# Performance work log

Measured on AMD Instinct MI355X. Metric: run time of the kernel, lower is better.

## Reference

```python
import jax, jax.numpy as jnp
import numpy as np

MAX_DISP = 40   # init kwarg max_disp
STRIDE_2 = 1    # init kwarg stride_2


def setup_inputs() -> dict:
    key = jax.random.key(0)
    k1, k2 = jax.random.split(key)
    B, C, H, W = 8, 128, 160, 320
    x_1 = jax.random.normal(k1, (B, C, H, W), dtype=jnp.float32)
    x_2 = jax.random.normal(k2, (B, C, H, W), dtype=jnp.float32)
    return {"x_1": x_1, "x_2": x_2}


def reference(x_1, x_2):
    # x_1, x_2: [B, C, H, W]
    pad = MAX_DISP * 2
    W = x_1.shape[3]
    # left-pad x_2 along width, matching F.pad(x_2, (pad, 0, 0, 0))
    x2p = jnp.pad(x_2, ((0, 0), (0, 0), (0, 0), (pad, 0)))
    # one [B,H,W] correlation map per displacement (small fixed set of 81 shifts)
    outs = [
        jnp.sum(x_1 * jax.lax.dynamic_slice_in_dim(x2p, d, W, axis=3), axis=1)
        for d in range(0, pad + 1, STRIDE_2)
    ]
    return jnp.stack(outs, axis=1)  # [B, D, H, W], D = 2*max_disp//stride + 1
```

## Files before the change

kernel.cpp:

```cpp
#include <hip/hip_runtime.h>


#define CB 8
#define CC 128
#define CH 160
#define CW 320
#define CD 81
#define CPAD 80
#define TW 160
#define NTHR 640
#define AROWS 160
#define BROWS 240
#define KC 64
#define ROWP 72
#define HW (CH*CW)

typedef __attribute__((ext_vector_type(8))) short short8;
typedef __attribute__((ext_vector_type(4))) float f32x4;

__device__ __forceinline__ unsigned pk2(float a, float b) {
    unsigned ua = __float_as_uint(a), ub = __float_as_uint(b);
    ua = (ua + 0x7fffu + ((ua >> 16) & 1u)) >> 16;
    ub = (ub + 0x7fffu + ((ub >> 16) & 1u)) >> 16;
    return ua | (ub << 16);
}

__global__ __launch_bounds__(NTHR, 5) void corr1d_mfma(
    const float* __restrict__ x1,
    const float* __restrict__ x2,
    float* __restrict__ out)
{
    __shared__ __align__(16) unsigned short lA[AROWS * ROWP];
    __shared__ __align__(16) unsigned short lB[BROWS * ROWP];

    const int tid = threadIdx.x;
    const int bid = blockIdx.x;
    const int wt = bid & 1;
    const int h  = (bid >> 1) % CH;
    const int b  = bid / (2 * CH);
    const int w0 = wt * TW;

    const int lane = tid & 63;
    const int s    = tid >> 6;
    const int n    = lane & 15;
    const int q    = lane >> 4;

    const float* x1p = x1 + ((size_t)b * CC * CH + (size_t)h) * CW;
    const float* x2p = x2 + ((size_t)b * CC * CH + (size_t)h) * CW;

    f32x4 acc[6];
#pragma unroll
    for (int t = 0; t < 6; t++) acc[t] = (f32x4){0.f, 0.f, 0.f, 0.f};

    for (int c0 = 0; c0 < CC; c0 += KC) {
        if (c0) __syncthreads();

#pragma unroll
        for (int j = 0; j < 3; j++) {
            int i = tid + j * NTHR;
            if (i < 1600) {
                int cq = i & 15;
                int rt = i >> 4;
                int kl = cq << 2;
                int c  = c0 + kl;
                float4 v[4];
                unsigned short* dst;
                if (rt < 40) {
                    int gw = w0 + (rt << 2);
                    const float* p = x1p + (size_t)c * HW + gw;
#pragma unroll
                    for (int cc = 0; cc < 4; cc++)
                        v[cc] = *(const float4*)(p + (size_t)cc * HW);
                    dst = &lA[(rt << 2) * ROWP + kl];
                } else {
                    int rb = rt - 40;
                    int gw = w0 - CPAD + (rb << 2);
                    if (gw >= 0) {
                        const float* p = x2p + (size_t)c * HW + gw;
#pragma unroll
                        for (int cc = 0; cc < 4; cc++)
                            v[cc] = *(const float4*)(p + (size_t)cc * HW);
                    } else {
#pragma unroll
                        for (int cc = 0; cc < 4; cc++)
                            v[cc] = make_float4(0.f, 0.f, 0.f, 0.f);
                    }
                    dst = &lB[(rb << 2) * ROWP + kl];
                }
                uint2 r0 = make_uint2(pk2(v[0].x, v[1].x), pk2(v[2].x, v[3].x));
                uint2 r1 = make_uint2(pk2(v[0].y, v[1].y), pk2(v[2].y, v[3].y));
                uint2 r2 = make_uint2(pk2(v[0].z, v[1].z), pk2(v[2].z, v[3].z));
                uint2 r3 = make_uint2(pk2(v[0].w, v[1].w), pk2(v[2].w, v[3].w));
                *(uint2*)(dst + 0 * ROWP) = r0;
                *(uint2*)(dst + 1 * ROWP) = r1;
                *(uint2*)(dst + 2 * ROWP) = r2;
                *(uint2*)(dst + 3 * ROWP) = r3;
            }
        }
        __syncthreads();

        const unsigned short* arow = &lA[(16 * s + n) * ROWP];
#pragma unroll
        for (int ko = 0; ko < KC; ko += 32) {
            short8 av = *(const short8*)(arow + ko + 8 * q);
#pragma unroll
            for (int t = 0; t < 6; t++) {
                short8 bv = *(const short8*)(&lB[(16 * (s + t) + n) * ROWP + ko + 8 * q]);
                acc[t] = __builtin_amdgcn_mfma_f32_16x16x32_bf16(av, bv, acc[t], 0, 0, 0);
            }
        }
    }

    float* op = out + ((size_t)b * CD * CH + (size_t)h) * CW + w0 + 16 * s;
#pragma unroll
    for (int t = 0; t < 6; t++) {
#pragma unroll
        for (int r = 0; r < 4; r++) {
            int m = 4 * q + r;
            int d = 16 * t + n - m;
            if (d >= 0 && d <= CPAD)
                op[(size_t)d * HW + m] = acc[t][r];
        }
    }
}

extern "C" void kernel_launch(void* const* d_in, const int* in_sizes, int n_in,
                              void* d_out, int out_size, void* d_ws, size_t ws_size,
                              hipStream_t stream) {
    const float* x1 = (const float*)d_in[0];
    const float* x2 = (const float*)d_in[1];
    float* out = (float*)d_out;
    dim3 grid(CB * CH * 2);
    dim3 block(NTHR);
    corr1d_mfma<<<grid, block, 0, stream>>>(x1, x2, out);
}
```

Measured before the change: 510.8 us.

## Shrink tiles, load x1 fragments directly to registers, remap blocks for locality

Cuts the width tile from 160 to 64 (256 threads, 5 tiles per row) and loads each wave's x1 A-fragments straight from global memory into registers, converted to bf16, so the A tile no longer goes through LDS. The blockIdx is remapped so that consecutive blocks spread across XCDs while neighbouring width tiles stay grouped. The manual round-to-nearest bf16 pack is replaced with the hardware v_cvt_pk_bf16_f32 instruction. In exchange, the x2 halo is reloaded more often relative to useful work (144 rows staged per 64 outputs instead of 240 per 160), and the direct A loads are uncoalesced scalar strided loads.

```diff
diff --git a/kernel.cpp b/kernel.cpp
--- a/kernel.cpp
+++ b/kernel.cpp
@@ -7,10 +7,10 @@
 #define CW 320
 #define CD 81
 #define CPAD 80
-#define TW 160
-#define NTHR 640
-#define AROWS 160
-#define BROWS 240
+#define TW 64
+#define NTHR 256
+#define BROWS 144
+#define NTILE 576
 #define KC 64
 #define ROWP 72
 #define HW (CH*CW)
@@ -18,26 +18,27 @@
 typedef __attribute__((ext_vector_type(8))) short short8;
 typedef __attribute__((ext_vector_type(4))) float f32x4;
 
-__device__ __forceinline__ unsigned pk2(float a, float b) {
-    unsigned ua = __float_as_uint(a), ub = __float_as_uint(b);
-    ua = (ua + 0x7fffu + ((ua >> 16) & 1u)) >> 16;
-    ub = (ub + 0x7fffu + ((ub >> 16) & 1u)) >> 16;
-    return ua | (ub << 16);
+__device__ __forceinline__ unsigned cvt_pk(float lo, float hi) {
+    unsigned r;
+    asm("v_cvt_pk_bf16_f32 %0, %1, %2" : "=v"(r) : "v"(lo), "v"(hi));
+    return r;
 }
 
-__global__ __launch_bounds__(NTHR, 5) void corr1d_mfma(
+__global__ __launch_bounds__(NTHR, 6) void corr1d_mfma(
     const float* __restrict__ x1,
     const float* __restrict__ x2,
     float* __restrict__ out)
 {
-    __shared__ __align__(16) unsigned short lA[AROWS * ROWP];
     __shared__ __align__(16) unsigned short lB[BROWS * ROWP];
 
     const int tid = threadIdx.x;
     const int bid = blockIdx.x;
-    const int wt = bid & 1;
-    const int h  = (bid >> 1) % CH;
-    const int b  = bid / (2 * CH);
+
+    const int v  = (bid & 7) * 800 + (bid >> 3);
+    const int g  = v / 5;
+    const int wt = v - 5 * g;
+    const int b  = g / CH;
+    const int h  = g - b * CH;
     const int w0 = wt * TW;
 
     const int lane = tid & 63;
@@ -48,64 +49,72 @@
     const float* x1p = x1 + ((size_t)b * CC * CH + (size_t)h) * CW;
     const float* x2p = x2 + ((size_t)b * CC * CH + (size_t)h) * CW;
 
+    short8 aF[4];
+    {
+        const float* ap = x1p + (size_t)(8 * q) * HW + (w0 + 16 * s + n);
+#pragma unroll
+        for (int kf = 0; kf < 4; kf++) {
+            const float* p = ap + (size_t)(32 * kf) * HW;
+            float f0 = p[0];
+            float f1 = p[(size_t)1 * HW];
+            float f2 = p[(size_t)2 * HW];
+            float f3 = p[(size_t)3 * HW];
+            float f4 = p[(size_t)4 * HW];
+            float f5 = p[(size_t)5 * HW];
+            float f6 = p[(size_t)6 * HW];
+            float f7 = p[(size_t)7 * HW];
+            union { unsigned u[4]; short8 v8; } cv;
+            cv.u[0] = cvt_pk(f0, f1);
+            cv.u[1] = cvt_pk(f2, f3);
+            cv.u[2] = cvt_pk(f4, f5);
+            cv.u[3] = cvt_pk(f6, f7);
+            aF[kf] = cv.v8;
+        }
+    }
+
     f32x4 acc[6];
 #pragma unroll
     for (int t = 0; t < 6; t++) acc[t] = (f32x4){0.f, 0.f, 0.f, 0.f};
 
-    for (int c0 = 0; c0 < CC; c0 += KC) {
-        if (c0) __syncthreads();
+#pragma unroll
+    for (int half = 0; half < 2; half++) {
+        const int c0 = half * KC;
+        if (half) __syncthreads();
 
 #pragma unroll
         for (int j = 0; j < 3; j++) {
-            int i = tid + j * NTHR;
-            if (i < 1600) {
-                int cq = i & 15;
-                int rt = i >> 4;
-                int kl = cq << 2;
-                int c  = c0 + kl;
-                float4 v[4];
-                unsigned short* dst;
-                if (rt < 40) {
-                    int gw = w0 + (rt << 2);
-                    const float* p = x1p + (size_t)c * HW + gw;
-#pragma unroll
-                    for (int cc = 0; cc < 4; cc++)
-                        v[cc] = *(const float4*)(p + (size_t)cc * HW);
-                    dst = &lA[(rt << 2) * ROWP + kl];
+            const int i = tid + j * NTHR;
+            if (i < NTILE) {
+                const int cq = i & 15;
+                const int rt = i >> 4;
+                const int kl = cq << 2;
+                const int gw = w0 - CPAD + (rt << 2);
+                float4 v0, v1, v2, v3;
+                if (gw >= 0) {
+                    const float* p = x2p + (size_t)(c0 + kl) * HW + gw;
+                    v0 = *(const float4*)(p);
+                    v1 = *(const float4*)(p + (size_t)1 * HW);
+                    v2 = *(const float4*)(p + (size_t)2 * HW);
+                    v3 = *(const float4*)(p + (size_t)3 * HW);
                 } else {
-                    int rb = rt - 40;
-                    int gw = w0 - CPAD + (rb << 2);
-                    if (gw >= 0) {
-                        const float* p = x2p + (size_t)c * HW + gw;
-#pragma unroll
-                        for (int cc = 0; cc < 4; cc++)
-                            v[cc] = *(const float4*)(p + (size_t)cc * HW);
-                    } else {
-#pragma unroll
-                        for (int cc = 0; cc < 4; cc++)
-                            v[cc] = make_float4(0.f, 0.f, 0.f, 0.f);
-                    }
-                    dst = &lB[(rb << 2) * ROWP + kl];
+                    v0 = v1 = v2 = v3 = make_float4(0.f, 0.f, 0.f, 0.f);
                 }
-                uint2 r0 = make_uint2(pk2(v[0].x, v[1].x), pk2(v[2].x, v[3].x));
-                uint2 r1 = make_uint2(pk2(v[0].y, v[1].y), pk2(v[2].y, v[3].y));
-                uint2 r2 = make_uint2(pk2(v[0].z, v[1].z), pk2(v[2].z, v[3].z));
-                uint2 r3 = make_uint2(pk2(v[0].w, v[1].w), pk2(v[2].w, v[3].w));
-                *(uint2*)(dst + 0 * ROWP) = r0;
-                *(uint2*)(dst + 1 * ROWP) = r1;
-                *(uint2*)(dst + 2 * ROWP) = r2;
-                *(uint2*)(dst + 3 * ROWP) = r3;
+                unsigned short* dst = &lB[(rt << 2) * ROWP + kl];
+                *(uint2*)(dst + 0 * ROWP) = make_uint2(cvt_pk(v0.x, v1.x), cvt_pk(v2.x, v3.x));
+                *(uint2*)(dst + 1 * ROWP) = make_uint2(cvt_pk(v0.y, v1.y), cvt_pk(v2.y, v3.y));
+                *(uint2*)(dst + 2 * ROWP) = make_uint2(cvt_pk(v0.z, v1.z), cvt_pk(v2.z, v3.z));
+                *(uint2*)(dst + 3 * ROWP) = make_uint2(cvt_pk(v0.w, v1.w), cvt_pk(v2.w, v3.w));
             }
         }
         __syncthreads();
 
-        const unsigned short* arow = &lA[(16 * s + n) * ROWP];
 #pragma unroll
-        for (int ko = 0; ko < KC; ko += 32) {
-            short8 av = *(const short8*)(arow + ko + 8 * q);
+        for (int ko = 0; ko < 2; ko++) {
+            const short8 av = aF[half * 2 + ko];
+            const unsigned short* bb = &lB[(size_t)n * ROWP + ko * 32 + 8 * q];
 #pragma unroll
             for (int t = 0; t < 6; t++) {
-                short8 bv = *(const short8*)(&lB[(16 * (s + t) + n) * ROWP + ko + 8 * q]);
+                short8 bv = *(const short8*)(bb + (size_t)(16 * (s + t)) * ROWP);
                 acc[t] = __builtin_amdgcn_mfma_f32_16x16x32_bf16(av, bv, acc[t], 0, 0, 0);
             }
         }
@@ -130,7 +139,7 @@
     const float* x1 = (const float*)d_in[0];
     const float* x2 = (const float*)d_in[1];
     float* out = (float*)d_out;
-    dim3 grid(CB * CH * 2);
+    dim3 grid(CB * CH * 5);
     dim3 block(NTHR);
     corr1d_mfma<<<grid, block, 0, stream>>>(x1, x2, out);
 }
```

After: 494.3 us. 1.03x faster.
